# Kernel tuning notes

Measured on AMD Instinct MI355X. Metric: run time of the kernel, lower is better.

Reference implementation:

```python
import jax, jax.numpy as jnp
import numpy as np

B, C, L, H, T, W = 512, 256, 256, 512, 16, 8  # batch, num_channels, seq_len, hidden_dim, timestep, windows


def setup_inputs() -> dict:
    key = jax.random.key(0)
    ks = jax.random.split(key, 8)
    s = 0.02
    return {
        "features_aug2": jax.random.normal(ks[0], (B, C, L), jnp.float32),
        "c_t": jax.random.normal(ks[1], (B, W, H), jnp.float32),
        "Wk_w": jax.random.normal(ks[2], (T, C, H), jnp.float32) * s,
        "Wk_b": jnp.zeros((T, C), jnp.float32),
        "pw1": jax.random.normal(ks[3], (C // 2, H), jnp.float32) * s,
        "pb1": jnp.zeros((C // 2,), jnp.float32),
        "bn_gamma": jnp.ones((C // 2,), jnp.float32),
        "bn_beta": jnp.zeros((C // 2,), jnp.float32),
        "pw2": jax.random.normal(ks[4], (C // 4, C // 2), jnp.float32) * s,
        "pb2": jnp.zeros((C // 4,), jnp.float32),
        "t_sample": 100,
    }


def reference(features_aug2, c_t, Wk_w, Wk_b, pw1, pb1, bn_gamma, bn_beta, pw2, pb2, t_sample):
    z2 = jnp.transpose(features_aug2, (0, 2, 1))            # [B, L, C]
    seq_len = z2.shape[1]
    Tn, Cn = Wk_w.shape[0], Wk_w.shape[1]
    Wn = c_t.shape[1]
    Bn = c_t.shape[0]

    # encode_samples: window slices of z_aug2 at offsets t+1 .. t+T (clipped to seq end)
    starts = jnp.minimum(t_sample + 1 + jnp.arange(Tn), seq_len - Wn)  # [T]
    idx = starts[:, None] + jnp.arange(Wn)                   # [T, W]
    encode = jnp.transpose(z2[:, idx, :], (1, 0, 2, 3))      # [T, B, W, C]

    # pred[i] = Wk[i](c_t): batched linear over all timesteps
    pred = jnp.einsum('bwh,tch->tbwc', c_t, Wk_w) + Wk_b[:, None, None, :]  # [T, B, W, C]

    # fused InfoNCE: all T*W pairwise (B x B) score matrices at once
    scores = jnp.einsum('tbwc,tawc->twba', encode, pred)     # [T, W, B, B]
    logp = jax.nn.log_softmax(scores, axis=-1)               # LogSoftmax over dim=1 of each [B,B] (torch implicit dim)
    diag = jnp.diagonal(logp, axis1=-2, axis2=-1)            # [T, W, B]
    nce = -jnp.sum(diag) / (Bn * Tn * Wn)

    # projection head on c_t.reshape(-1, H): Linear -> BatchNorm1d (train stats) -> ReLU -> Linear
    x = c_t.reshape(-1, c_t.shape[-1])                       # [B*W, H]
    h1 = x @ pw1.T + pb1                                     # [B*W, C/2]
    mean = jnp.mean(h1, axis=0)
    var = jnp.mean((h1 - mean) ** 2, axis=0)                 # biased variance (BN train mode)
    h1 = (h1 - mean) * jax.lax.rsqrt(var + 1e-5) * bn_gamma + bn_beta
    h1 = jax.nn.relu(h1)
    proj = h1 @ pw2.T + pb2                                  # [B*W, C/4]
    return nce, proj
```

## Files before the change

### kernel.cpp

```cpp
#include <hip/hip_runtime.h>

#define B_SZ 512
#define C_CH 256
#define L_SEQ 256
#define H_DIM 512
#define T_STEP 16
#define W_WIN 8
#define NSLAB 24
#define NCE_SHIFT 40.0f

typedef __attribute__((ext_vector_type(8))) short short8;
typedef __attribute__((ext_vector_type(4))) float f32x4;

#define GLOBAL_U32 const __attribute__((address_space(1))) unsigned int*
#define LDS_U32 __attribute__((address_space(3))) unsigned int*
#define ASYNC_COPY16(g, l) \
  __builtin_amdgcn_global_load_lds((GLOBAL_U32)(const void*)(g), (LDS_U32)(void*)(l), 16, 0, 0)

__device__ inline unsigned short f2bf(float x) {
  unsigned u = __float_as_uint(x);
  u = (u + 0x7FFFu + ((u >> 16) & 1u)) >> 16;
  return (unsigned short)u;
}

__global__ __launch_bounds__(256) void prep(const float* __restrict__ ct,
                                            const float* __restrict__ wk,
                                            const float* __restrict__ pw1,
                                            unsigned short* __restrict__ ctb,
                                            unsigned short* __restrict__ wkb,
                                            unsigned short* __restrict__ pw1b,
                                            float* __restrict__ bnp1,
                                            float* __restrict__ bnp2,
                                            float* __restrict__ out) {
  int b = blockIdx.x;
  if (b == 4160) {
    if (threadIdx.x < 128) { bnp1[threadIdx.x] = 0.f; bnp2[threadIdx.x] = 0.f; }
    if (threadIdx.x == 0) out[0] = 0.f;
    return;
  }
  const float* s;
  unsigned short* d;
  int base;
  if (b < 2048)      { s = ct;  d = ctb;  base = b * 1024; }
  else if (b < 4096) { s = wk;  d = wkb;  base = (b - 2048) * 1024; }
  else               { s = pw1; d = pw1b; base = (b - 4096) * 1024; }
  int i = base + threadIdx.x * 4;
  float4 v = ((const float4*)s)[i >> 2];
  ushort4 o;
  o.x = f2bf(v.x); o.y = f2bf(v.y); o.z = f2bf(v.z); o.w = f2bf(v.w);
  ((ushort4*)d)[i >> 2] = o;
}

__global__ __launch_bounds__(256) void build_slabs2(const float* __restrict__ f,
                                                    unsigned short* __restrict__ F,
                                                    const int* __restrict__ tsp) {
  const int ts = tsp[0];
  const int lmin = min(ts + 1, L_SEQ - W_WIN);
  const int b = blockIdx.x;
  const int c = threadIdx.x;
  const float* src = f + ((size_t)b * C_CH + c) * L_SEQ;
  float v[NSLAB];
#pragma unroll
  for (int lp = 0; lp < NSLAB; lp++) {
    int l = lmin + lp;
    v[lp] = (l < L_SEQ) ? src[l] : 0.f;
  }
#pragma unroll
  for (int lp = 0; lp < NSLAB; lp++)
    F[((size_t)lp * B_SZ + b) * C_CH + c] = f2bf(v[lp]);
}

template <int MODE>
__global__ __launch_bounds__(256) void gemm_bt(const unsigned short* __restrict__ A,
                                               const unsigned short* __restrict__ Bt,
                                               const float* __restrict__ bias,
                                               unsigned short* __restrict__ outb,
                                               float* __restrict__ outf,
                                               float* __restrict__ bnp1,
                                               float* __restrict__ bnp2, int K) {
  __shared__ __align__(16) unsigned short As[128 * 64];
  __shared__ __align__(16) unsigned short Bs[128 * 64];
  const int tid = threadIdx.x;
  const int wv = tid >> 6, lane = tid & 63, quad = lane >> 4, l15 = lane & 15;
  const int wm = wv >> 1, wn = wv & 1;
  int M0, N0;
  if (MODE == 0) {
    int swz = (blockIdx.x & 7) * 128 + (blockIdx.x >> 3);
    M0 = (swz >> 5) * 128;
    N0 = (swz & 31) * 128;
  } else {
    M0 = blockIdx.x * 128;
    N0 = 0;
  }

  f32x4 acc[4][4];
#pragma unroll
  for (int i = 0; i < 4; i++)
#pragma unroll
    for (int j = 0; j < 4; j++) acc[i][j] = (f32x4){0.f, 0.f, 0.f, 0.f};

  for (int k0 = 0; k0 < K; k0 += 64) {
#pragma unroll
    for (int i = 0; i < 4; i++) {
      int chunk = (i * 4 + wv) * 64 + lane;
      int row = chunk >> 3, off = chunk & 7;
      const unsigned short* ga = A + (size_t)(M0 + row) * K + k0 + off * 8;
      const unsigned short* gb = Bt + (size_t)(N0 + row) * K + k0 + off * 8;
      ASYNC_COPY16(ga, &As[(size_t)(i * 4 + wv) * 512]);
      ASYNC_COPY16(gb, &Bs[(size_t)(i * 4 + wv) * 512]);
    }
    __syncthreads();
#pragma unroll
    for (int kk = 0; kk < 64; kk += 32) {
      short8 af[4], bfr[4];
#pragma unroll
      for (int i = 0; i < 4; i++)
        af[i] = *(const short8*)&As[(wm * 64 + i * 16 + l15) * 64 + kk + quad * 8];
#pragma unroll
      for (int j = 0; j < 4; j++)
        bfr[j] = *(const short8*)&Bs[(wn * 64 + j * 16 + l15) * 64 + kk + quad * 8];
#pragma unroll
      for (int i = 0; i < 4; i++)
#pragma unroll
        for (int j = 0; j < 4; j++)
          acc[i][j] = __builtin_amdgcn_mfma_f32_16x16x32_bf16(af[i], bfr[j], acc[i][j], 0, 0, 0);
    }
    __syncthreads();
  }

  float st1[4], st2[4];
#pragma unroll
  for (int j = 0; j < 4; j++) { st1[j] = 0.f; st2[j] = 0.f; }
#pragma unroll
  for (int i = 0; i < 4; i++) {
    int rbase = M0 + wm * 64 + i * 16 + quad * 4;
#pragma unroll
    for (int j = 0; j < 4; j++) {
      int cc = N0 + wn * 64 + j * 16 + l15;
      float bv = bias[cc];
#pragma unroll
      for (int r = 0; r < 4; r++) {
        int rr = rbase + r;
        float v = acc[i][j][r] + bv;
        if (MODE == 0) {
          int t = cc >> 8, c = cc & 255, a = rr >> 3, w_ = rr & 7;
          outb[((size_t)(t * 8 + w_) * 512 + a) * 256 + c] = f2bf(v);
        } else {
          outf[(size_t)rr * 128 + cc] = v;
          st1[j] += v;
          st2[j] += v * v;
        }
      }
    }
  }
  if (MODE == 1) {
    __shared__ float red1[2][128], red2[2][128];
#pragma unroll
    for (int j = 0; j < 4; j++) {
      float a1 = st1[j], a2 = st2[j];
      a1 += __shfl_xor(a1, 16); a1 += __shfl_xor(a1, 32);
      a2 += __shfl_xor(a2, 16); a2 += __shfl_xor(a2, 32);
      if (quad == 0) {
        red1[wm][wn * 64 + j * 16 + l15] = a1;
        red2[wm][wn * 64 + j * 16 + l15] = a2;
      }
    }
    __syncthreads();
    if (tid < 128) {
      atomicAdd(&bnp1[tid], red1[0][tid] + red1[1][tid]);
      atomicAdd(&bnp2[tid], red2[0][tid] + red2[1][tid]);
    }
  }
}

__global__ __launch_bounds__(256) void scores_gemm(const unsigned short* __restrict__ F,
                                                   const unsigned short* __restrict__ pred,
                                                   const int* __restrict__ tsp,
                                                   float* __restrict__ rowsum_p,
                                                   float* __restrict__ diagv) {
  __shared__ __align__(16) unsigned short As[128 * 64];
  __shared__ __align__(16) unsigned short Bs[128 * 64];
  const int tid = threadIdx.x;
  const int wv = tid >> 6, lane = tid & 63, quad = lane >> 4, l15 = lane & 15;
  const int wm = wv >> 1, wn = wv & 1;
  const int swz = (blockIdx.x & 7) * 256 + (blockIdx.x >> 3);
  const int tw = swz >> 4, rowblk = (swz >> 2) & 3, colblk = swz & 3;
  const int t = tw >> 3, w_ = tw & 7;
  const int ts = tsp[0];
  const int lmin = min(ts + 1, L_SEQ - W_WIN);
  const int lp = min(ts + 1 + t, L_SEQ - W_WIN) + w_ - lmin;
  const unsigned short* A = F + (size_t)lp * (B_SZ * C_CH) + (size_t)rowblk * 128 * C_CH;
  const unsigned short* Bt = pred + (size_t)tw * (B_SZ * C_CH) + (size_t)colblk * 128 * C_CH;

  f32x4 acc[4][4];
#pragma unroll
  for (int i = 0; i < 4; i++)
#pragma unroll
    for (int j = 0; j < 4; j++) acc[i][j] = (f32x4){0.f, 0.f, 0.f, 0.f};

  for (int k0 = 0; k0 < C_CH; k0 += 64) {
#pragma unroll
    for (int i = 0; i < 4; i++) {
      int chunk = (i * 4 + wv) * 64 + lane;
      int row = chunk >> 3, off = chunk & 7;
      ASYNC_COPY16(A + (size_t)row * C_CH + k0 + off * 8, &As[(size_t)(i * 4 + wv) * 512]);
      ASYNC_COPY16(Bt + (size_t)row * C_CH + k0 + off * 8, &Bs[(size_t)(i * 4 + wv) * 512]);
    }
    __syncthreads();
#pragma unroll
    for (int kk = 0; kk < 64; kk += 32) {
      short8 af[4], bfr[4];
#pragma unroll
      for (int i = 0; i < 4; i++)
        af[i] = *(const short8*)&As[(wm * 64 + i * 16 + l15) * 64 + kk + quad * 8];
#pragma unroll
      for (int j = 0; j < 4; j++)
        bfr[j] = *(const short8*)&Bs[(wn * 64 + j * 16 + l15) * 64 + kk + quad * 8];
#pragma unroll
      for (int i = 0; i < 4; i++)
#pragma unroll
        for (int j = 0; j < 4; j++)
          acc[i][j] = __builtin_amdgcn_mfma_f32_16x16x32_bf16(af[i], bfr[j], acc[i][j], 0, 0, 0);
    }
    __syncthreads();
  }

#pragma unroll
  for (int i = 0; i < 4; i++) {
#pragma unroll
    for (int r = 0; r < 4; r++) {
      float e = 0.f;
#pragma unroll
      for (int j = 0; j < 4; j++) e += __expf(acc[i][j][r] - NCE_SHIFT);
      e += __shfl_xor(e, 1);
      e += __shfl_xor(e, 2);
      e += __shfl_xor(e, 4);
      e += __shfl_xor(e, 8);
      if (l15 == 0) {
        int b = rowblk * 128 + wm * 64 + i * 16 + quad * 4 + r;
        rowsum_p[((size_t)tw * 8 + colblk * 2 + wn) * B_SZ + b] = e;
      }
    }
  }
  if (rowblk == colblk && wm == wn) {
#pragma unroll
    for (int i = 0; i < 4; i++)
#pragma unroll
      for (int r = 0; r < 4; r++)
        if (l15 == quad * 4 + r) {
          int b = rowblk * 128 + wm * 64 + i * 16 + quad * 4 + r;
          diagv[(size_t)tw * B_SZ + b] = acc[i][i][r];
        }
  }
}

__global__ __launch_bounds__(256) void nce_rows(const float* __restrict__ rowsum_p,
                                                const float* __restrict__ diagv,
                                                float* __restrict__ out) {
  int gid = blockIdx.x * 256 + threadIdx.x;
  float s = 0.f;
  for (int i = gid; i < 65536; i += 16384) {
    int tw = i >> 9, b = i & 511;
    float rs = 0.f;
#pragma unroll
    for (int p = 0; p < 8; p++) rs += rowsum_p[((size_t)tw * 8 + p) * B_SZ + b];
    s += logf(rs) + NCE_SHIFT - diagv[i];
  }
#pragma unroll
  for (int off = 1; off < 64; off <<= 1) s += __shfl_xor(s, off);
  __shared__ float r[4];
  if ((threadIdx.x & 63) == 0) r[threadIdx.x >> 6] = s;
  __syncthreads();
  if (threadIdx.x == 0)
    atomicAdd(out, (r[0] + r[1] + r[2] + r[3]) * (1.f / 65536.f));
}

__global__ __launch_bounds__(256) void proj2(const float* __restrict__ h1,
                                             const float* __restrict__ bnp1,
                                             const float* __restrict__ bnp2,
                                             const float* __restrict__ g,
                                             const float* __restrict__ bta,
                                             const float* __restrict__ pw2,
                                             const float* __restrict__ pb2,
                                             float* __restrict__ out) {
  __shared__ float hsT[128][68];
  __shared__ float pw2T[128][68];
  __shared__ float scs[128], shs[128];
  const int tid = threadIdx.x;
  for (int idx = tid; idx < 64 * 128; idx += 256) {
    int oc = idx >> 7, k = idx & 127;
    pw2T[k][oc] = pw2[idx];
  }
  if (tid < 128) {
    float mean = bnp1[tid] * (1.f / 4096.f);
    float var = bnp2[tid] * (1.f / 4096.f) - mean * mean;
    float scale = g[tid] * rsqrtf(var + 1e-5f);
    scs[tid] = scale;
    shs[tid] = bta[tid] - mean * scale;
  }
  __syncthreads();
  const int r0 = blockIdx.x * 64;
  for (int idx = tid; idx < 64 * 128; idx += 256) {
    int r = idx >> 7, k = idx & 127;
    float v = h1[(size_t)(r0 + r) * 128 + k];
    hsT[k][r] = fmaxf(v * scs[k] + shs[k], 0.f);
  }
  __syncthreads();
  const int tx = tid & 15, ty = tid >> 4;
  float acc[4][4] = {};
  for (int k = 0; k < 128; k++) {
    f32x4 hv = *(const f32x4*)&hsT[k][ty * 4];
    f32x4 wv = *(const f32x4*)&pw2T[k][tx * 4];
#pragma unroll
    for (int i = 0; i < 4; i++)
#pragma unroll
      for (int j = 0; j < 4; j++) acc[i][j] += hv[i] * wv[j];
  }
#pragma unroll
  for (int i = 0; i < 4; i++) {
    int rr = r0 + ty * 4 + i;
#pragma unroll
    for (int j = 0; j < 4; j++)
      out[(size_t)rr * 64 + tx * 4 + j] = acc[i][j] + pb2[tx * 4 + j];
  }
}

extern "C" void kernel_launch(void* const* d_in, const int* in_sizes, int n_in,
                              void* d_out, int out_size, void* d_ws, size_t ws_size,
                              hipStream_t stream) {
  const float* features = (const float*)d_in[0];
  const float* c_t      = (const float*)d_in[1];
  const float* Wk_w     = (const float*)d_in[2];
  const float* Wk_b     = (const float*)d_in[3];
  const float* pw1      = (const float*)d_in[4];
  const float* pb1      = (const float*)d_in[5];
  const float* bn_gamma = (const float*)d_in[6];
  const float* bn_beta  = (const float*)d_in[7];
  const float* pw2      = (const float*)d_in[8];
  const float* pb2      = (const float*)d_in[9];
  const int*   tsp      = (const int*)d_in[10];
  float* out = (float*)d_out;

  char* ws = (char*)d_ws;
  size_t off = 0;
  auto carve = [&](size_t bytes) { void* p = ws + off; off += (bytes + 255) & ~(size_t)255; return p; };
  unsigned short* ct_bf  = (unsigned short*)carve((size_t)4096 * 512 * 2);
  unsigned short* wk_bf  = (unsigned short*)carve((size_t)4096 * 512 * 2);
  unsigned short* pw1_bf = (unsigned short*)carve((size_t)128 * 512 * 2);
  unsigned short* F      = (unsigned short*)carve((size_t)NSLAB * 512 * 256 * 2);
  unsigned short* pred   = (unsigned short*)carve((size_t)16 * 8 * 512 * 256 * 2);
  float* h1       = (float*)carve((size_t)4096 * 128 * 4);
  float* bnp1     = (float*)carve((size_t)128 * 4);
  float* bnp2     = (float*)carve((size_t)128 * 4);
  float* rowsum_p = (float*)carve((size_t)128 * 8 * 512 * 4);
  float* diagv    = (float*)carve((size_t)65536 * 4);

  prep<<<4161, 256, 0, stream>>>(c_t, Wk_w, pw1, ct_bf, wk_bf, pw1_bf, bnp1, bnp2, out);
  build_slabs2<<<512, 256, 0, stream>>>(features, F, tsp);

  gemm_bt<0><<<1024, 256, 0, stream>>>(ct_bf, wk_bf, Wk_b, pred, nullptr, nullptr, nullptr, 512);
  gemm_bt<1><<<32, 256, 0, stream>>>(ct_bf, pw1_bf, pb1, nullptr, h1, bnp1, bnp2, 512);

  scores_gemm<<<2048, 256, 0, stream>>>(F, pred, tsp, rowsum_p, diagv);
  nce_rows<<<64, 256, 0, stream>>>(rowsum_p, diagv, out);

  proj2<<<64, 256, 0, stream>>>(h1, bnp1, bnp2, bn_gamma, bn_beta, pw2, pb2, out + 1);
}
```

Measured before the change: 296.8 us.

## Use 256x256 double-buffered pipelined GEMM core for pred and scores kernels

Replaces the 128x128 single-buffered GEMMs for the pred projection and the pairwise score matrices with a shared 256x256-tile, 8-wave core. It double-buffers LDS with async global-to-LDS copies, swizzles LDS addresses, interleaves staging with MFMA phases and raises wave priority during MFMA. The pred epilogue now stages the output through LDS and writes it with vectorized 16-byte stores instead of scattered 2-byte stores. The aim is to hide load latency behind compute and raise data reuse, at the cost of larger LDS use, fewer blocks and hand-placed waitcnt counts that must stay correct.

```diff
diff --git a/kernel.cpp b/kernel.cpp
--- a/kernel.cpp
+++ b/kernel.cpp
@@ -16,6 +16,10 @@
 #define LDS_U32 __attribute__((address_space(3))) unsigned int*
 #define ASYNC_COPY16(g, l) \
   __builtin_amdgcn_global_load_lds((GLOBAL_U32)(const void*)(g), (LDS_U32)(void*)(l), 16, 0, 0)
+
+#define BARRIER __builtin_amdgcn_s_barrier()
+#define SCHEDB  __builtin_amdgcn_sched_barrier(0)
+#define LGK0 do { asm volatile("s_waitcnt lgkmcnt(0)" ::: "memory"); __builtin_amdgcn_sched_barrier(0); } while (0)
 
 __device__ inline unsigned short f2bf(float x) {
   unsigned u = __float_as_uint(x);
@@ -70,11 +74,177 @@
     F[((size_t)lp * B_SZ + b) * C_CH + c] = f2bf(v[lp]);
 }
 
-template <int MODE>
-__global__ __launch_bounds__(256) void gemm_bt(const unsigned short* __restrict__ A,
+#define PHASE(BUF, H, MH, STAGE_STMT) do {                                              \
+    const int hb_ = ((BUF) * 2 + (H)) * 8192;                                           \
+    short8 af_[4];                                                                      \
+    _Pragma("unroll") for (int mq = 0; mq < 4; mq++)                                    \
+      af_[mq] = *(const short8*)&Al[hb_ + abase + ((MH) * 4 + mq) * 512];               \
+    if ((MH) == 0) {                                                                    \
+      _Pragma("unroll") for (int n = 0; n < 4; n++)                                     \
+        bf[n] = *(const short8*)&Bl[hb_ + bbase + n * 512];                             \
+    }                                                                                   \
+    STAGE_STMT;                                                                         \
+    BARRIER;                                                                            \
+    LGK0;                                                                               \
+    __builtin_amdgcn_s_setprio(1);                                                      \
+    _Pragma("unroll") for (int mq = 0; mq < 4; mq++)                                    \
+    _Pragma("unroll") for (int n = 0; n < 4; n++)                                       \
+      acc[(MH) * 4 + mq][n] =                                                           \
+          __builtin_amdgcn_mfma_f32_16x16x32_bf16(af_[mq], bf[n], acc[(MH)*4+mq][n], 0, 0, 0); \
+    __builtin_amdgcn_s_setprio(0);                                                      \
+  } while (0)
+
+template <int NT>
+__device__ __forceinline__ void gemm256(unsigned short* Al, unsigned short* Bl,
+                                        const unsigned short* __restrict__ A,
+                                        const unsigned short* __restrict__ B,
+                                        int Kst, f32x4 (&acc)[8][4]) {
+  const int tid = threadIdx.x;
+  const int wv = tid >> 6, lane = tid & 63, quad = lane >> 4, l15 = lane & 15;
+  const int wm = wv >> 2, wn = wv & 3;
+  const int qsw = (lane & 3) ^ ((lane >> 2) & 3);
+  const int qs8 = (quad ^ (l15 & 3)) * 8;
+  const int abase = (wm * 128 + l15) * 32 + qs8;
+  const int bbase = (wn * 64 + l15) * 32 + qs8;
+
+  auto stage = [&](int buf, int h, int kt) {
+    const int kc = kt * 64 + h * 32 + qsw * 8;
+#pragma unroll
+    for (int i = 0; i < 2; i++) {
+      int g = wv + i * 8;
+      int row = g * 16 + (lane >> 2);
+      ASYNC_COPY16(A + (size_t)row * Kst + kc, Al + ((buf * 2 + h) * 8192) + g * 512);
+      ASYNC_COPY16(B + (size_t)row * Kst + kc, Bl + ((buf * 2 + h) * 8192) + g * 512);
+    }
+  };
+
+  short8 bf[4];
+  stage(0, 0, 0); stage(0, 1, 0); stage(1, 0, 1); stage(1, 1, 1);
+  asm volatile("s_waitcnt vmcnt(8)" ::: "memory");
+  BARRIER; SCHEDB;
+
+  for (int k = 0; k < NT; k++) {
+    const int cur = k & 1;
+    PHASE(cur, 0, 0, { if (k >= 1 && k + 1 < NT) stage((k + 1) & 1, 1, k + 1); });
+    BARRIER; SCHEDB;
+    PHASE(cur, 0, 1, {});
+    BARRIER; SCHEDB;
+    PHASE(cur, 1, 0, { if (k + 2 < NT) stage(cur, 0, k + 2); });
+    BARRIER; SCHEDB;
+    PHASE(cur, 1, 1, {});
+    if (k < NT - 2)       asm volatile("s_waitcnt vmcnt(4)" ::: "memory");
+    else if (k == NT - 2) asm volatile("s_waitcnt vmcnt(0)" ::: "memory");
+    BARRIER; SCHEDB;
+  }
+}
+
+__global__ __launch_bounds__(512, 2) void pred_gemm(const unsigned short* __restrict__ A,
+                                                    const unsigned short* __restrict__ Bt,
+                                                    const float* __restrict__ bias,
+                                                    unsigned short* __restrict__ pred) {
+  __shared__ unsigned short Al[32768];
+  __shared__ unsigned short Bl[32768];
+  const int tid = threadIdx.x;
+  const int wv = tid >> 6, lane = tid & 63, quad = lane >> 4, l15 = lane & 15;
+  const int wm = wv >> 2, wn = wv & 3;
+  const int M0 = (blockIdx.x >> 4) * 256, N0 = (blockIdx.x & 15) * 256;
+
+  f32x4 acc[8][4];
+#pragma unroll
+  for (int m = 0; m < 8; m++)
+#pragma unroll
+    for (int n = 0; n < 4; n++) acc[m][n] = (f32x4){0.f, 0.f, 0.f, 0.f};
+
+  gemm256<8>(Al, Bl, A + (size_t)M0 * 512, Bt + (size_t)N0 * 512, 512, acc);
+
+  float bvs[4];
+#pragma unroll
+  for (int n = 0; n < 4; n++) bvs[n] = bias[N0 + wn * 64 + n * 16 + l15];
+  unsigned short* cstash = wm ? Bl : Al;
+#pragma unroll
+  for (int m = 0; m < 8; m++)
+#pragma unroll
+    for (int n = 0; n < 4; n++) {
+      int cc = wn * 64 + n * 16 + l15;
+#pragma unroll
+      for (int r = 0; r < 4; r++) {
+        int rl = (m * 16 + quad * 4 + r);
+        cstash[rl * 256 + cc] = f2bf(acc[m][n][r] + bvs[n]);
+      }
+    }
+  BARRIER;
+  const int tq = N0 >> 8, a0 = M0 >> 3;
+  for (int idx = tid; idx < 256 * 32; idx += 512) {
+    int rl = idx >> 5, seg = idx & 31;
+    short8 v = *(const short8*)((rl < 128 ? Al : Bl) + (rl & 127) * 256 + seg * 8);
+    int a = a0 + (rl >> 3), w_ = rl & 7;
+    *(short8*)&pred[(((size_t)tq * 8 + w_) * 512 + a) * 256 + seg * 8] = v;
+  }
+}
+
+__global__ __launch_bounds__(512, 2) void scores_gemm(const unsigned short* __restrict__ F,
+                                                      const unsigned short* __restrict__ pred,
+                                                      const int* __restrict__ tsp,
+                                                      float* __restrict__ rowsum_p,
+                                                      float* __restrict__ diagv) {
+  __shared__ unsigned short Al[32768];
+  __shared__ unsigned short Bl[32768];
+  const int tid = threadIdx.x;
+  const int wv = tid >> 6, lane = tid & 63, quad = lane >> 4, l15 = lane & 15;
+  const int wm = wv >> 2, wn = wv & 3;
+  const int swz = (blockIdx.x & 7) * 64 + (blockIdx.x >> 3);
+  const int tw = swz >> 2, rb = (swz >> 1) & 1, cb = swz & 1;
+  const int t = tw >> 3, w_ = tw & 7;
+  const int ts = tsp[0];
+  const int lmin = min(ts + 1, L_SEQ - W_WIN);
+  const int lp = min(ts + 1 + t, L_SEQ - W_WIN) + w_ - lmin;
+  const unsigned short* A = F + (size_t)lp * (B_SZ * C_CH) + (size_t)rb * 256 * C_CH;
+  const unsigned short* Bt = pred + (size_t)tw * (B_SZ * C_CH) + (size_t)cb * 256 * C_CH;
+
+  f32x4 acc[8][4];
+#pragma unroll
+  for (int m = 0; m < 8; m++)
+#pragma unroll
+    for (int n = 0; n < 4; n++) acc[m][n] = (f32x4){0.f, 0.f, 0.f, 0.f};
+
+  gemm256<4>(Al, Bl, A, Bt, 256, acc);
+
+#pragma unroll
+  for (int m = 0; m < 8; m++) {
+#pragma unroll
+    for (int r = 0; r < 4; r++) {
+      float e = 0.f;
+#pragma unroll
+      for (int n = 0; n < 4; n++) e += __expf(acc[m][n][r] - NCE_SHIFT);
+      e += __shfl_xor(e, 1);
+      e += __shfl_xor(e, 2);
+      e += __shfl_xor(e, 4);
+      e += __shfl_xor(e, 8);
+      if (l15 == 0) {
+        int b = rb * 256 + wm * 128 + m * 16 + quad * 4 + r;
+        rowsum_p[((size_t)tw * 8 + cb * 4 + wn) * B_SZ + b] = e;
+      }
+    }
+  }
+  if (rb == cb) {
+#pragma unroll
+    for (int m = 0; m < 8; m++)
+#pragma unroll
+      for (int n = 0; n < 4; n++)
+#pragma unroll
+        for (int r = 0; r < 4; r++) {
+          int d = wm * 128 + m * 16 + quad * 4 + r - wn * 64 - n * 16;
+          if (d == l15) {
+            int b = rb * 256 + wm * 128 + m * 16 + quad * 4 + r;
+            diagv[(size_t)tw * B_SZ + b] = acc[m][n][r];
+          }
+        }
+  }
+}
+
+__global__ __launch_bounds__(256) void gemm_h1(const unsigned short* __restrict__ A,
                                                const unsigned short* __restrict__ Bt,
                                                const float* __restrict__ bias,
-                                               unsigned short* __restrict__ outb,
                                                float* __restrict__ outf,
                                                float* __restrict__ bnp1,
                                                float* __restrict__ bnp2, int K) {
@@ -83,15 +253,7 @@
   const int tid = threadIdx.x;
   const int wv = tid >> 6, lane = tid & 63, quad = lane >> 4, l15 = lane & 15;
   const int wm = wv >> 1, wn = wv & 1;
-  int M0, N0;
-  if (MODE == 0) {
-    int swz = (blockIdx.x & 7) * 128 + (blockIdx.x >> 3);
-    M0 = (swz >> 5) * 128;
-    N0 = (swz & 31) * 128;
-  } else {
-    M0 = blockIdx.x * 128;
-    N0 = 0;
-  }
+  const int M0 = blockIdx.x * 128, N0 = 0;
 
   f32x4 acc[4][4];
 #pragma unroll
@@ -104,10 +266,8 @@
     for (int i = 0; i < 4; i++) {
       int chunk = (i * 4 + wv) * 64 + lane;
       int row = chunk >> 3, off = chunk & 7;
-      const unsigned short* ga = A + (size_t)(M0 + row) * K + k0 + off * 8;
-      const unsigned short* gb = Bt + (size_t)(N0 + row) * K + k0 + off * 8;
-      ASYNC_COPY16(ga, &As[(size_t)(i * 4 + wv) * 512]);
-      ASYNC_COPY16(gb, &Bs[(size_t)(i * 4 + wv) * 512]);
+      ASYNC_COPY16(A + (size_t)(M0 + row) * K + k0 + off * 8, &As[(size_t)(i * 4 + wv) * 512]);
+      ASYNC_COPY16(Bt + (size_t)(N0 + row) * K + k0 + off * 8, &Bs[(size_t)(i * 4 + wv) * 512]);
     }
     __syncthreads();
 #pragma unroll
@@ -136,121 +296,33 @@
     int rbase = M0 + wm * 64 + i * 16 + quad * 4;
 #pragma unroll
     for (int j = 0; j < 4; j++) {
-      int cc = N0 + wn * 64 + j * 16 + l15;
+      int cc = wn * 64 + j * 16 + l15;
       float bv = bias[cc];
 #pragma unroll
       for (int r = 0; r < 4; r++) {
         int rr = rbase + r;
         float v = acc[i][j][r] + bv;
-        if (MODE == 0) {
-          int t = cc >> 8, c = cc & 255, a = rr >> 3, w_ = rr & 7;
-          outb[((size_t)(t * 8 + w_) * 512 + a) * 256 + c] = f2bf(v);
-        } else {
-          outf[(size_t)rr * 128 + cc] = v;
-          st1[j] += v;
-          st2[j] += v * v;
-        }
+        outf[(size_t)rr * 128 + cc] = v;
+        st1[j] += v;
+        st2[j] += v * v;
       }
     }
   }
-  if (MODE == 1) {
-    __shared__ float red1[2][128], red2[2][128];
-#pragma unroll
-    for (int j = 0; j < 4; j++) {
-      float a1 = st1[j], a2 = st2[j];
-      a1 += __shfl_xor(a1, 16); a1 += __shfl_xor(a1, 32);
-      a2 += __shfl_xor(a2, 16); a2 += __shfl_xor(a2, 32);
-      if (quad == 0) {
-        red1[wm][wn * 64 + j * 16 + l15] = a1;
-        red2[wm][wn * 64 + j * 16 + l15] = a2;
-      }
-    }
-    __syncthreads();
-    if (tid < 128) {
-      atomicAdd(&bnp1[tid], red1[0][tid] + red1[1][tid]);
-      atomicAdd(&bnp2[tid], red2[0][tid] + red2[1][tid]);
-    }
-  }
-}
-
-__global__ __launch_bounds__(256) void scores_gemm(const unsigned short* __restrict__ F,
-                                                   const unsigned short* __restrict__ pred,
-                                                   const int* __restrict__ tsp,
-                                                   float* __restrict__ rowsum_p,
-                                                   float* __restrict__ diagv) {
-  __shared__ __align__(16) unsigned short As[128 * 64];
-  __shared__ __align__(16) unsigned short Bs[128 * 64];
-  const int tid = threadIdx.x;
-  const int wv = tid >> 6, lane = tid & 63, quad = lane >> 4, l15 = lane & 15;
-  const int wm = wv >> 1, wn = wv & 1;
-  const int swz = (blockIdx.x & 7) * 256 + (blockIdx.x >> 3);
-  const int tw = swz >> 4, rowblk = (swz >> 2) & 3, colblk = swz & 3;
-  const int t = tw >> 3, w_ = tw & 7;
-  const int ts = tsp[0];
-  const int lmin = min(ts + 1, L_SEQ - W_WIN);
-  const int lp = min(ts + 1 + t, L_SEQ - W_WIN) + w_ - lmin;
-  const unsigned short* A = F + (size_t)lp * (B_SZ * C_CH) + (size_t)rowblk * 128 * C_CH;
-  const unsigned short* Bt = pred + (size_t)tw * (B_SZ * C_CH) + (size_t)colblk * 128 * C_CH;
-
-  f32x4 acc[4][4];
-#pragma unroll
-  for (int i = 0; i < 4; i++)
-#pragma unroll
-    for (int j = 0; j < 4; j++) acc[i][j] = (f32x4){0.f, 0.f, 0.f, 0.f};
-
-  for (int k0 = 0; k0 < C_CH; k0 += 64) {
-#pragma unroll
-    for (int i = 0; i < 4; i++) {
-      int chunk = (i * 4 + wv) * 64 + lane;
-      int row = chunk >> 3, off = chunk & 7;
-      ASYNC_COPY16(A + (size_t)row * C_CH + k0 + off * 8, &As[(size_t)(i * 4 + wv) * 512]);
-      ASYNC_COPY16(Bt + (size_t)row * C_CH + k0 + off * 8, &Bs[(size_t)(i * 4 + wv) * 512]);
-    }
-    __syncthreads();
-#pragma unroll
-    for (int kk = 0; kk < 64; kk += 32) {
-      short8 af[4], bfr[4];
-#pragma unroll
-      for (int i = 0; i < 4; i++)
-        af[i] = *(const short8*)&As[(wm * 64 + i * 16 + l15) * 64 + kk + quad * 8];
-#pragma unroll
-      for (int j = 0; j < 4; j++)
-        bfr[j] = *(const short8*)&Bs[(wn * 64 + j * 16 + l15) * 64 + kk + quad * 8];
-#pragma unroll
-      for (int i = 0; i < 4; i++)
-#pragma unroll
-        for (int j = 0; j < 4; j++)
-          acc[i][j] = __builtin_amdgcn_mfma_f32_16x16x32_bf16(af[i], bfr[j], acc[i][j], 0, 0, 0);
-    }
-    __syncthreads();
-  }
-
-#pragma unroll
-  for (int i = 0; i < 4; i++) {
-#pragma unroll
-    for (int r = 0; r < 4; r++) {
-      float e = 0.f;
-#pragma unroll
-      for (int j = 0; j < 4; j++) e += __expf(acc[i][j][r] - NCE_SHIFT);
-      e += __shfl_xor(e, 1);
-      e += __shfl_xor(e, 2);
-      e += __shfl_xor(e, 4);
-      e += __shfl_xor(e, 8);
-      if (l15 == 0) {
-        int b = rowblk * 128 + wm * 64 + i * 16 + quad * 4 + r;
-        rowsum_p[((size_t)tw * 8 + colblk * 2 + wn) * B_SZ + b] = e;
-      }
-    }
-  }
-  if (rowblk == colblk && wm == wn) {
-#pragma unroll
-    for (int i = 0; i < 4; i++)
-#pragma unroll
-      for (int r = 0; r < 4; r++)
-        if (l15 == quad * 4 + r) {
-          int b = rowblk * 128 + wm * 64 + i * 16 + quad * 4 + r;
-          diagv[(size_t)tw * B_SZ + b] = acc[i][i][r];
-        }
+  __shared__ float red1[2][128], red2[2][128];
+#pragma unroll
+  for (int j = 0; j < 4; j++) {
+    float a1 = st1[j], a2 = st2[j];
+    a1 += __shfl_xor(a1, 16); a1 += __shfl_xor(a1, 32);
+    a2 += __shfl_xor(a2, 16); a2 += __shfl_xor(a2, 32);
+    if (quad == 0) {
+      red1[wm][wn * 64 + j * 16 + l15] = a1;
+      red2[wm][wn * 64 + j * 16 + l15] = a2;
+    }
+  }
+  __syncthreads();
+  if (tid < 128) {
+    atomicAdd(&bnp1[tid], red1[0][tid] + red1[1][tid]);
+    atomicAdd(&bnp2[tid], red2[0][tid] + red2[1][tid]);
   }
 }
 
@@ -358,10 +430,10 @@
   prep<<<4161, 256, 0, stream>>>(c_t, Wk_w, pw1, ct_bf, wk_bf, pw1_bf, bnp1, bnp2, out);
   build_slabs2<<<512, 256, 0, stream>>>(features, F, tsp);
 
-  gemm_bt<0><<<1024, 256, 0, stream>>>(ct_bf, wk_bf, Wk_b, pred, nullptr, nullptr, nullptr, 512);
-  gemm_bt<1><<<32, 256, 0, stream>>>(ct_bf, pw1_bf, pb1, nullptr, h1, bnp1, bnp2, 512);
-
-  scores_gemm<<<2048, 256, 0, stream>>>(F, pred, tsp, rowsum_p, diagv);
+  pred_gemm<<<256, 512, 0, stream>>>(ct_bf, wk_bf, Wk_b, pred);
+  gemm_h1<<<32, 256, 0, stream>>>(ct_bf, pw1_bf, pb1, h1, bnp1, bnp2, 512);
+
+  scores_gemm<<<512, 512, 0, stream>>>(F, pred, tsp, rowsum_p, diagv);
   nce_rows<<<64, 256, 0, stream>>>(rowsum_p, diagv, out);
 
   proj2<<<64, 256, 0, stream>>>(h1, bnp1, bnp2, bn_gamma, bn_beta, pw2, pb2, out + 1);
```

After: 287.3 us, median of 2. 3.2% less time.
